# Performance work log

Measured on AMD Instinct MI355X. Metric: run time of the kernel, lower is better.

Reference implementation:

```python
import jax, jax.numpy as jnp
import numpy as np

USER_NUM = 100000
ITEM_NUM = 100000
DIM = 64
BS = 256


def setup_inputs() -> dict:
    key = jax.random.key(0)
    k1, k2, k3, k4, k5 = jax.random.split(key, 5)
    # xavier_normal-ish scale for embeddings/linear
    user_table = jax.random.normal(k1, (USER_NUM, DIM), dtype=jnp.float32) * 0.1
    item_table = jax.random.normal(k2, (ITEM_NUM, DIM), dtype=jnp.float32) * 0.1
    cls_w = jax.random.normal(k3, (5, DIM), dtype=jnp.float32) * (2.0 / (DIM + 5)) ** 0.5
    cls_b = jnp.zeros((5,), dtype=jnp.float32)
    batch_user = jax.random.randint(k4, (BS,), 0, USER_NUM, dtype=jnp.int64)
    values = jnp.array([[1.0, 2.0, 3.0, 4.0, 5.0]], dtype=jnp.float32)
    return {
        "batch_user": batch_user,
        "user_table": user_table,
        "item_table": item_table,
        "cls_w": cls_w,
        "cls_b": cls_b,
        "values": values,
    }


def reference(batch_user, user_table, item_table, cls_w, cls_b, values):
    # forward_full_items: score every (user, item) pair.
    # Torch materializes h_ui = (u repeated) * (items tiled) of shape
    # [bs*item_num, dim]; mathematically logits = einsum over dim, so we
    # fuse the broadcasted product with the tiny Linear to avoid the
    # huge expanded intermediate while computing identical math.
    u = user_table[batch_user]                       # [bs, dim]
    # logits[b,i,c] = sum_d u[b,d] * item[i,d] * W[c,d] + b[c]
    logits = jnp.einsum('bd,id,cd->bic', u, item_table, cls_w) + cls_b  # [bs, item_num, 5]
    prob = jax.nn.softmax(logits, axis=-1)
    return jnp.sum(prob * values[0], axis=-1)        # [bs, item_num]
```

## Files before the change

### kernel.cpp

```cpp
#include <hip/hip_runtime.h>

#define I_TOTAL 100000
#define DIM 64
#define BS 256

typedef __attribute__((ext_vector_type(8))) short bf16x8;
typedef __attribute__((ext_vector_type(4))) float f32x4;

__device__ inline unsigned short f2bf(float x) {
    union { float f; unsigned u; } v; v.f = x;
    return (unsigned short)((v.u + 0x8000u) >> 16);
}

__global__ __launch_bounds__(256) void prep_M(
    const int* __restrict__ bu, const float* __restrict__ ut,
    const float* __restrict__ cw, unsigned short* __restrict__ Mbf)
{
    int idx = blockIdx.x * 256 + threadIdx.x;
    int d = (idx & 15) * 4;
    int n = idx >> 4;
    int c = n >> 8, b = n & 255;
    const float s = 1.4426950408889634f;
    float4 u = *(const float4*)(ut + (long)bu[b] * DIM + d);
    float4 w = *(const float4*)(cw + c * DIM + d);
    ushort4 r;
    r.x = f2bf(u.x * w.x * s);
    r.y = f2bf(u.y * w.y * s);
    r.z = f2bf(u.z * w.z * s);
    r.w = f2bf(u.w * w.w * s);
    *(ushort4*)(Mbf + n * DIM + d) = r;
}

__global__ __launch_bounds__(256) void conv_items(
    const float* __restrict__ item, unsigned short* __restrict__ itbf)
{
    long t = (long)blockIdx.x * 256 + threadIdx.x;
    const float4* p = (const float4*)(item + t * 8);
    float4 a = p[0], b = p[1];
    ushort4 r0, r1;
    r0.x = f2bf(a.x); r0.y = f2bf(a.y); r0.z = f2bf(a.z); r0.w = f2bf(a.w);
    r1.x = f2bf(b.x); r1.y = f2bf(b.y); r1.z = f2bf(b.z); r1.w = f2bf(b.w);
    ushort4* q = (ushort4*)(itbf + t * 8);
    q[0] = r0; q[1] = r1;
}

__global__ __launch_bounds__(256) void gemm_softmax(
    const unsigned short* __restrict__ itbf,
    const unsigned short* __restrict__ Mbf,
    const float* __restrict__ clsb, const float* __restrict__ vals,
    float* __restrict__ out)
{
    const int blk = blockIdx.x;
    const int r8 = blk & 7;
    const int q  = blk >> 3;
    const int g  = q & 15;
    const int a  = q >> 4;
    const int y  = a * 8 + r8;
    if (y >= 98) return;

    const int lane = threadIdx.x & 63;
    const int wave = threadIdx.x >> 6;
    const int col  = lane & 15;
    const int quad = lane >> 4;

    const int b_base = g * 16;
    const int i_base = y * 1024 + wave * 256;

    bf16x8 afr[5][2];
#pragma unroll
    for (int c = 0; c < 5; ++c) {
        const unsigned short* p = Mbf + (c * BS + b_base + col) * DIM + quad * 8;
        afr[c][0] = *(const bf16x8*)p;
        afr[c][1] = *(const bf16x8*)(p + 32);
    }

    const f32x4 zero = (f32x4){0.f, 0.f, 0.f, 0.f};

    const float s = 1.4426950408889634f;
    float bb[5], vv[5];
#pragma unroll
    for (int c = 0; c < 5; ++c) { bb[c] = clsb[c] * s; vv[c] = vals[c]; }

    if (y < 97) {
        float* op[4];
#pragma unroll
        for (int rr = 0; rr < 4; ++rr)
            op[rr] = out + (size_t)(b_base + quad * 4 + rr) * I_TOTAL + (i_base + col);

        const unsigned short* bp = itbf + (size_t)(i_base + col) * DIM + quad * 8;

#pragma unroll 1
        for (int t4 = 0; t4 < 4; ++t4) {
#pragma unroll
            for (int ti = 0; ti < 4; ++ti) {
                bf16x8 b0 = *(const bf16x8*)(bp + ti * 1024);
                bf16x8 b1 = *(const bf16x8*)(bp + ti * 1024 + 32);
                f32x4 acc[5];
#pragma unroll
                for (int c = 0; c < 5; ++c) {
                    acc[c] = __builtin_amdgcn_mfma_f32_16x16x32_bf16(afr[c][0], b0, zero, 0, 0, 0);
                    acc[c] = __builtin_amdgcn_mfma_f32_16x16x32_bf16(afr[c][1], b1, acc[c], 0, 0, 0);
                }
#pragma unroll
                for (int rr = 0; rr < 4; ++rr) {
                    float e0 = exp2f(acc[0][rr] + bb[0]);
                    float e1 = exp2f(acc[1][rr] + bb[1]);
                    float e2 = exp2f(acc[2][rr] + bb[2]);
                    float e3 = exp2f(acc[3][rr] + bb[3]);
                    float e4 = exp2f(acc[4][rr] + bb[4]);
                    float den = ((e0 + e1) + (e2 + e3)) + e4;
                    float num = e0 * vv[0];
                    num = fmaf(e1, vv[1], num);
                    num = fmaf(e2, vv[2], num);
                    num = fmaf(e3, vv[3], num);
                    num = fmaf(e4, vv[4], num);
                    op[rr][ti * 16] = num * __builtin_amdgcn_rcpf(den);
                }
            }
            bp += 4 * 1024;
#pragma unroll
            for (int rr = 0; rr < 4; ++rr) op[rr] += 64;
        }
    } else {
#pragma unroll 1
        for (int t = 0; t < 16; ++t) {
            int i  = i_base + t * 16 + col;
            int ic = i < I_TOTAL ? i : I_TOTAL - 1;
            const unsigned short* p2 = itbf + (size_t)ic * DIM + quad * 8;
            bf16x8 b0 = *(const bf16x8*)p2;
            bf16x8 b1 = *(const bf16x8*)(p2 + 32);
            f32x4 acc[5];
#pragma unroll
            for (int c = 0; c < 5; ++c) {
                acc[c] = __builtin_amdgcn_mfma_f32_16x16x32_bf16(afr[c][0], b0, zero, 0, 0, 0);
                acc[c] = __builtin_amdgcn_mfma_f32_16x16x32_bf16(afr[c][1], b1, acc[c], 0, 0, 0);
            }
            if (i < I_TOTAL) {
#pragma unroll
                for (int rr = 0; rr < 4; ++rr) {
                    float e0 = exp2f(acc[0][rr] + bb[0]);
                    float e1 = exp2f(acc[1][rr] + bb[1]);
                    float e2 = exp2f(acc[2][rr] + bb[2]);
                    float e3 = exp2f(acc[3][rr] + bb[3]);
                    float e4 = exp2f(acc[4][rr] + bb[4]);
                    float den = ((e0 + e1) + (e2 + e3)) + e4;
                    float num = e0 * vv[0];
                    num = fmaf(e1, vv[1], num);
                    num = fmaf(e2, vv[2], num);
                    num = fmaf(e3, vv[3], num);
                    num = fmaf(e4, vv[4], num);
                    out[(size_t)(b_base + quad * 4 + rr) * I_TOTAL + i] =
                        num * __builtin_amdgcn_rcpf(den);
                }
            }
        }
    }
}

__global__ __launch_bounds__(256) void gemm_softmax_fb(
    const float* __restrict__ item, const unsigned short* __restrict__ Mbf,
    const float* __restrict__ clsb, const float* __restrict__ vals,
    float* __restrict__ out)
{
    const int lane = threadIdx.x & 63;
    const int wave = threadIdx.x >> 6;
    const int col  = lane & 15;
    const int quad = lane >> 4;
    const int  b_base = blockIdx.x * 16;
    const long i_wave = (long)blockIdx.y * 256 + wave * 64;

    bf16x8 afr[5][2];
#pragma unroll
    for (int c = 0; c < 5; ++c) {
        const unsigned short* p = Mbf + (c * BS + b_base + col) * DIM + quad * 8;
        afr[c][0] = *(const bf16x8*)p;
        afr[c][1] = *(const bf16x8*)(p + 32);
    }
    f32x4 acc[5][4];
#pragma unroll
    for (int c = 0; c < 5; ++c)
#pragma unroll
        for (int t = 0; t < 4; ++t) acc[c][t] = (f32x4){0.f,0.f,0.f,0.f};
#pragma unroll
    for (int t = 0; t < 4; ++t) {
        long i  = i_wave + t * 16 + col;
        long ic = (i < I_TOTAL) ? i : (I_TOTAL - 1);
        const float4* fp = (const float4*)(item + ic * DIM);
        float4 q0 = fp[2*quad], q1 = fp[2*quad+1], q2 = fp[8+2*quad], q3 = fp[8+2*quad+1];
        bf16x8 b0, b1;
        b0[0]=(short)f2bf(q0.x); b0[1]=(short)f2bf(q0.y); b0[2]=(short)f2bf(q0.z); b0[3]=(short)f2bf(q0.w);
        b0[4]=(short)f2bf(q1.x); b0[5]=(short)f2bf(q1.y); b0[6]=(short)f2bf(q1.z); b0[7]=(short)f2bf(q1.w);
        b1[0]=(short)f2bf(q2.x); b1[1]=(short)f2bf(q2.y); b1[2]=(short)f2bf(q2.z); b1[3]=(short)f2bf(q2.w);
        b1[4]=(short)f2bf(q3.x); b1[5]=(short)f2bf(q3.y); b1[6]=(short)f2bf(q3.z); b1[7]=(short)f2bf(q3.w);
#pragma unroll
        for (int c = 0; c < 5; ++c) {
            acc[c][t] = __builtin_amdgcn_mfma_f32_16x16x32_bf16(afr[c][0], b0, acc[c][t], 0, 0, 0);
            acc[c][t] = __builtin_amdgcn_mfma_f32_16x16x32_bf16(afr[c][1], b1, acc[c][t], 0, 0, 0);
        }
    }
    const float s = 1.4426950408889634f;
    float bb[5], vv[5];
#pragma unroll
    for (int c = 0; c < 5; ++c) { bb[c] = clsb[c] * s; vv[c] = vals[c]; }
#pragma unroll
    for (int t = 0; t < 4; ++t) {
        long i = i_wave + t * 16 + col;
        if (i >= I_TOTAL) continue;
#pragma unroll
        for (int r = 0; r < 4; ++r) {
            int b = b_base + quad * 4 + r;
            float num = 0.f, den = 0.f;
#pragma unroll
            for (int c = 0; c < 5; ++c) {
                float e = exp2f(acc[c][t][r] + bb[c]);
                den += e; num = fmaf(e, vv[c], num);
            }
            out[(long)b * I_TOTAL + i] = num * __builtin_amdgcn_rcpf(den);
        }
    }
}

extern "C" void kernel_launch(void* const* d_in, const int* in_sizes, int n_in,
                              void* d_out, int out_size, void* d_ws, size_t ws_size,
                              hipStream_t stream) {
    const int*   bu   = (const int*)d_in[0];
    const float* ut   = (const float*)d_in[1];
    const float* it   = (const float*)d_in[2];
    const float* cw   = (const float*)d_in[3];
    const float* cb   = (const float*)d_in[4];
    const float* vals = (const float*)d_in[5];
    float* out = (float*)d_out;
    unsigned short* Mbf  = (unsigned short*)d_ws;
    unsigned short* itbf = (unsigned short*)((char*)d_ws + 163840);

    const size_t needed = 163840 + (size_t)I_TOTAL * DIM * 2;

    prep_M<<<80, 256, 0, stream>>>(bu, ut, cw, Mbf);
    if (ws_size >= needed) {
        conv_items<<<3125, 256, 0, stream>>>(it, itbf);
        gemm_softmax<<<1664, 256, 0, stream>>>(itbf, Mbf, cb, vals, out);
    } else {
        dim3 grid(16, 391);
        gemm_softmax_fb<<<grid, 256, 0, stream>>>(it, Mbf, cb, vals, out);
    }
}
```

Measured before the change: 187.1 us.

## Stage softmax outputs through LDS for vectorized stores and use hardware exp2

Each wave writes its per-tile results into a private LDS region, then reads them back transposed so every lane stores four contiguous floats with a 128-bit global store instead of scattered scalar stores. The goal is more efficient write coalescing for the large output. Separately, exp2f is replaced by the raw hardware exp2 builtin, which drops the range/denormal handling wrappers. It adds LDS traffic and relies on intra-wave ordering without explicit barriers.

```diff
diff --git a/kernel.cpp b/kernel.cpp
--- a/kernel.cpp
+++ b/kernel.cpp
@@ -50,6 +50,8 @@
     const float* __restrict__ clsb, const float* __restrict__ vals,
     float* __restrict__ out)
 {
+    __shared__ float ldsb[4224];
+
     const int blk = blockIdx.x;
     const int r8 = blk & 7;
     const int q  = blk >> 3;
@@ -75,17 +77,19 @@
     }
 
     const f32x4 zero = (f32x4){0.f, 0.f, 0.f, 0.f};
-
     const float s = 1.4426950408889634f;
     float bb[5], vv[5];
 #pragma unroll
     for (int c = 0; c < 5; ++c) { bb[c] = clsb[c] * s; vv[c] = vals[c]; }
 
     if (y < 97) {
+        float* wlds = ldsb + wave * 1056 + quad * 264 + col;
+        const float* rlds = ldsb + wave * 1056 + quad * 264 + 4 * col;
+
         float* op[4];
 #pragma unroll
-        for (int rr = 0; rr < 4; ++rr)
-            op[rr] = out + (size_t)(b_base + quad * 4 + rr) * I_TOTAL + (i_base + col);
+        for (int k = 0; k < 4; ++k)
+            op[k] = out + (size_t)(b_base + quad * 4 + k) * I_TOTAL + (i_base + 4 * col);
 
         const unsigned short* bp = itbf + (size_t)(i_base + col) * DIM + quad * 8;
 
@@ -101,25 +105,32 @@
                     acc[c] = __builtin_amdgcn_mfma_f32_16x16x32_bf16(afr[c][0], b0, zero, 0, 0, 0);
                     acc[c] = __builtin_amdgcn_mfma_f32_16x16x32_bf16(afr[c][1], b1, acc[c], 0, 0, 0);
                 }
+                f32x4 l[5];
+#pragma unroll
+                for (int c = 0; c < 5; ++c) l[c] = acc[c] + bb[c];
 #pragma unroll
                 for (int rr = 0; rr < 4; ++rr) {
-                    float e0 = exp2f(acc[0][rr] + bb[0]);
-                    float e1 = exp2f(acc[1][rr] + bb[1]);
-                    float e2 = exp2f(acc[2][rr] + bb[2]);
-                    float e3 = exp2f(acc[3][rr] + bb[3]);
-                    float e4 = exp2f(acc[4][rr] + bb[4]);
+                    float e0 = __builtin_amdgcn_exp2f(l[0][rr]);
+                    float e1 = __builtin_amdgcn_exp2f(l[1][rr]);
+                    float e2 = __builtin_amdgcn_exp2f(l[2][rr]);
+                    float e3 = __builtin_amdgcn_exp2f(l[3][rr]);
+                    float e4 = __builtin_amdgcn_exp2f(l[4][rr]);
                     float den = ((e0 + e1) + (e2 + e3)) + e4;
                     float num = e0 * vv[0];
                     num = fmaf(e1, vv[1], num);
                     num = fmaf(e2, vv[2], num);
                     num = fmaf(e3, vv[3], num);
                     num = fmaf(e4, vv[4], num);
-                    op[rr][ti * 16] = num * __builtin_amdgcn_rcpf(den);
+                    wlds[rr * 64 + ti * 16] = num * __builtin_amdgcn_rcpf(den);
                 }
             }
+#pragma unroll
+            for (int k = 0; k < 4; ++k) {
+                f32x4 o4 = *(const f32x4*)(rlds + k * 64);
+                *(f32x4*)op[k] = o4;
+                op[k] += 64;
+            }
             bp += 4 * 1024;
-#pragma unroll
-            for (int rr = 0; rr < 4; ++rr) op[rr] += 64;
         }
     } else {
 #pragma unroll 1
@@ -138,11 +149,11 @@
             if (i < I_TOTAL) {
 #pragma unroll
                 for (int rr = 0; rr < 4; ++rr) {
-                    float e0 = exp2f(acc[0][rr] + bb[0]);
-                    float e1 = exp2f(acc[1][rr] + bb[1]);
-                    float e2 = exp2f(acc[2][rr] + bb[2]);
-                    float e3 = exp2f(acc[3][rr] + bb[3]);
-                    float e4 = exp2f(acc[4][rr] + bb[4]);
+                    float e0 = __builtin_amdgcn_exp2f(acc[0][rr] + bb[0]);
+                    float e1 = __builtin_amdgcn_exp2f(acc[1][rr] + bb[1]);
+                    float e2 = __builtin_amdgcn_exp2f(acc[2][rr] + bb[2]);
+                    float e3 = __builtin_amdgcn_exp2f(acc[3][rr] + bb[3]);
+                    float e4 = __builtin_amdgcn_exp2f(acc[4][rr] + bb[4]);
                     float den = ((e0 + e1) + (e2 + e3)) + e4;
                     float num = e0 * vv[0];
                     num = fmaf(e1, vv[1], num);
@@ -212,7 +223,7 @@
             float num = 0.f, den = 0.f;
 #pragma unroll
             for (int c = 0; c < 5; ++c) {
-                float e = exp2f(acc[c][t][r] + bb[c]);
+                float e = __builtin_amdgcn_exp2f(acc[c][t][r] + bb[c]);
                 den += e; num = fmaf(e, vv[c], num);
             }
             out[(long)b * I_TOTAL + i] = num * __builtin_amdgcn_rcpf(den);
```

After: 177.7 us. 5.0% less time.
